# Performance work log

Hardware: AMD Instinct MI355X
Metric: run time of the kernel (lower is better)

The kernel has to match this reference:

```python
import jax, jax.numpy as jnp
import numpy as np

# Multi-scale feature pyramid (static: determines per-level slice bounds)
SPATIAL_SHAPES = np.array([[100, 100], [50, 50], [25, 25], [13, 13], [7, 7]])  # (H, W) per level
LEVEL_START = np.concatenate([[0], np.cumsum(SPATIAL_SHAPES[:, 0] * SPATIAL_SHAPES[:, 1])])[:-1]
C = 256       # hidden_inplanes
HEADS = 8     # head_nums
POINTS = 4    # point_nums
LEVELS = 5    # feature_level_nums
FF = 2048     # feedforward_planes
DH = C // HEADS


def setup_inputs() -> dict:
    key = jax.random.key(0)
    ks = jax.random.split(key, 16)
    B = 2
    L = int((SPATIAL_SHAPES[:, 0] * SPATIAL_SHAPES[:, 1]).sum())  # 13343 tokens
    s = 0.02
    return {
        'src': jax.random.normal(ks[0], (B, L, C), jnp.float32),
        'pos': jax.random.normal(ks[1], (B, L, C), jnp.float32) * 0.1,
        'reference_points': jax.random.uniform(ks[2], (B, L, LEVELS, 2), jnp.float32),
        'wv': jax.random.normal(ks[3], (C, C), jnp.float32) * s,
        'bv': jnp.zeros((C,), jnp.float32),
        'wo': jax.random.normal(ks[4], (C, HEADS * LEVELS * POINTS * 2), jnp.float32) * s,
        'bo': jax.random.normal(ks[5], (HEADS * LEVELS * POINTS * 2,), jnp.float32) * 0.5,
        'wa': jax.random.normal(ks[6], (C, HEADS * LEVELS * POINTS), jnp.float32) * s,
        'ba': jnp.zeros((HEADS * LEVELS * POINTS,), jnp.float32),
        'wout': jax.random.normal(ks[7], (C, C), jnp.float32) * s,
        'bout': jnp.zeros((C,), jnp.float32),
        'ln1g': jnp.ones((C,), jnp.float32),
        'ln1b': jnp.zeros((C,), jnp.float32),
        'w1': jax.random.normal(ks[8], (C, FF), jnp.float32) * s,
        'b1': jnp.zeros((FF,), jnp.float32),
        'w2': jax.random.normal(ks[9], (FF, C), jnp.float32) * s,
        'b2': jnp.zeros((C,), jnp.float32),
        'ln2g': jnp.ones((C,), jnp.float32),
        'ln2b': jnp.zeros((C,), jnp.float32),
    }


def layernorm(x, g, b, eps=1e-5):
    m = jnp.mean(x, -1, keepdims=True)
    v = jnp.var(x, -1, keepdims=True)
    return (x - m) * jax.lax.rsqrt(v + eps) * g + b


def bilinear_sample(val, loc, Hs, Ws):
    # val: [B, heads, H*W, dh]   loc: [B, heads, Lq, P, 2] normalized coords in [0,1]
    # grid_sample semantics, align_corners=False, zero padding outside
    px = loc[..., 0] * Ws - 0.5
    py = loc[..., 1] * Hs - 0.5
    x0 = jnp.floor(px); y0 = jnp.floor(py)
    lx = px - x0;       ly = py - y0
    x0i = x0.astype(jnp.int32); y0i = y0.astype(jnp.int32)
    gather = jax.vmap(jax.vmap(lambda v, i: v[i]))  # over batch, head dims
    out = jnp.zeros(loc.shape[:-1] + (val.shape[-1],), val.dtype)
    for dx, dy, w in ((0, 0, (1 - lx) * (1 - ly)), (1, 0, lx * (1 - ly)),
                      (0, 1, (1 - lx) * ly), (1, 1, lx * ly)):
        xi = x0i + dx; yi = y0i + dy
        valid = (xi >= 0) & (xi < Ws) & (yi >= 0) & (yi < Hs)
        idx = jnp.clip(yi, 0, Hs - 1) * Ws + jnp.clip(xi, 0, Ws - 1)
        g = gather(val, idx)  # [B, heads, Lq, P, dh]
        out = out + (w * valid)[..., None] * g
    return out


def msdeform_attn(query, value_in, ref, wv, bv, wo, bo, wa, ba, wout, bout):
    B, Lq, _ = query.shape
    # value projection -> [B, heads, Len, dh]
    value = (value_in @ wv + bv).reshape(B, -1, HEADS, DH).transpose(0, 2, 1, 3)
    offsets = (query @ wo + bo).reshape(B, Lq, HEADS, LEVELS, POINTS, 2)
    attn = jax.nn.softmax((query @ wa + ba).reshape(B, Lq, HEADS, LEVELS * POINTS), -1)
    attn = attn.reshape(B, Lq, HEADS, LEVELS, POINTS)
    # offset normalizer = (W, H) per level
    norml = jnp.asarray(SPATIAL_SHAPES[:, ::-1].copy(), jnp.float32)
    loc = ref[:, :, None, :, None, :] + offsets / norml[None, None, None, :, None, :]
    acc = jnp.zeros((B, Lq, HEADS, DH), query.dtype)
    for l in range(LEVELS):
        Hs, Ws = int(SPATIAL_SHAPES[l, 0]), int(SPATIAL_SHAPES[l, 1])
        s = int(LEVEL_START[l])
        vl = value[:, :, s:s + Hs * Ws, :]
        locl = jnp.transpose(loc[:, :, :, l], (0, 2, 1, 3, 4))  # [B, heads, Lq, P, 2]
        samp = bilinear_sample(vl, locl, Hs, Ws)                 # [B, heads, Lq, P, dh]
        acc = acc + jnp.einsum('bhqpd,bqhp->bqhd', samp, attn[:, :, :, l])
    return acc.reshape(B, Lq, C) @ wout + bout


def reference(src, pos, reference_points, wv, bv, wo, bo, wa, ba, wout, bout,
              ln1g, ln1b, w1, b1, w2, b2, ln2g, ln2b):
    # DeformableTransformerEncoderLayer (eval mode, dropout off)
    q = src + pos
    src2 = msdeform_attn(q, src, reference_points, wv, bv, wo, bo, wa, ba, wout, bout)
    x = layernorm(src + src2, ln1g, ln1b)
    ffn = jax.nn.relu(x @ w1 + b1) @ w2 + b2
    return layernorm(x + ffn, ln2g, ln2b)
```

## Files before the change

kernel.cpp:

```cpp
#include <hip/hip_runtime.h>
#include <hip/hip_bf16.h>

typedef __hip_bfloat16 bf16;
typedef unsigned short ushort_t;
typedef __attribute__((ext_vector_type(8))) short bf16x8;
typedef __attribute__((ext_vector_type(16))) float f32x16;

__device__ __forceinline__ float us2f(unsigned short u) {
    unsigned int x = ((unsigned int)u) << 16;
    return __uint_as_float(x);
}
__device__ __forceinline__ ushort_t f2us(float f) {
    return ((__hip_bfloat16_raw)__float2bfloat16(f)).x;
}

__device__ __forceinline__ void gl_lds16(const ushort_t* g, ushort_t* l) {
    __builtin_amdgcn_global_load_lds(
        (const __attribute__((address_space(1))) void*)g,
        (__attribute__((address_space(3))) void*)l, 16, 0, 0);
}

template<bool RELU, bool OUT_BF16, bool HAS_RESID>
__device__ __forceinline__ void epi_store_tile(
    float* __restrict__ tl, const f32x16& acc, int lane,
    int mbase, int nbase, const float* __restrict__ bias,
    const float* __restrict__ resid, void* __restrict__ outv, int M, int N)
{
    const int l32 = lane & 31, hi = lane >> 5;
    #pragma unroll
    for (int r = 0; r < 16; ++r) {
        const int row = (r & 3) + ((r >> 2) << 3) + hi * 4;
        tl[row * 34 + l32] = acc[r];
    }
    const int rr = lane >> 1;
    const int cc = (lane & 1) * 16;
    const int m  = mbase + rr;
    const int nb = nbase + cc;
    if (m >= M || nb >= N) return;

    if (OUT_BF16) {
        bf16* op = (bf16*)outv + (size_t)m * N + nb;
        #pragma unroll
        for (int gv = 0; gv < 2; ++gv) {
            unsigned pk[4];
            #pragma unroll
            for (int q = 0; q < 2; ++q) {
                const int c = cc + gv * 8 + q * 4;
                const float4 v  = *reinterpret_cast<const float4*>(&tl[rr * 34 + c]);
                const float4 b4 = *reinterpret_cast<const float4*>(&bias[nbase + c]);
                float o0 = v.x + b4.x, o1 = v.y + b4.y;
                float o2 = v.z + b4.z, o3 = v.w + b4.w;
                if (HAS_RESID) {
                    const float4 r4 = *reinterpret_cast<const float4*>(
                        &resid[(size_t)m * N + nbase + c]);
                    o0 += r4.x; o1 += r4.y; o2 += r4.z; o3 += r4.w;
                }
                if (RELU) {
                    o0 = fmaxf(o0, 0.f); o1 = fmaxf(o1, 0.f);
                    o2 = fmaxf(o2, 0.f); o3 = fmaxf(o3, 0.f);
                }
                pk[q * 2 + 0] = (unsigned)f2us(o0) | ((unsigned)f2us(o1) << 16);
                pk[q * 2 + 1] = (unsigned)f2us(o2) | ((unsigned)f2us(o3) << 16);
            }
            int4 w4; w4.x = pk[0]; w4.y = pk[1]; w4.z = pk[2]; w4.w = pk[3];
            *reinterpret_cast<int4*>(op + gv * 8) = w4;
        }
    } else {
        float* op = (float*)outv + (size_t)m * N + nb;
        #pragma unroll
        for (int q = 0; q < 4; ++q) {
            const int c = cc + q * 4;
            const float4 v  = *reinterpret_cast<const float4*>(&tl[rr * 34 + c]);
            const float4 b4 = *reinterpret_cast<const float4*>(&bias[nbase + c]);
            float4 o;
            o.x = v.x + b4.x; o.y = v.y + b4.y;
            o.z = v.z + b4.z; o.w = v.w + b4.w;
            if (HAS_RESID) {
                const float4 r4 = *reinterpret_cast<const float4*>(
                    &resid[(size_t)m * N + nbase + c]);
                o.x += r4.x; o.y += r4.y; o.z += r4.z; o.w += r4.w;
            }
            if (RELU) {
                o.x = fmaxf(o.x, 0.f); o.y = fmaxf(o.y, 0.f);
                o.z = fmaxf(o.z, 0.f); o.w = fmaxf(o.w, 0.f);
            }
            *reinterpret_cast<float4*>(op + q * 4) = o;
        }
    }
}

__global__ __launch_bounds__(256) void cast2_kernel(
    const float* __restrict__ src, const float* __restrict__ pos,
    bf16* __restrict__ src_b, bf16* __restrict__ q_b, int n)
{
    int i = (blockIdx.x * 256 + threadIdx.x) * 4;
    if (i < n) {
        const float4 s4 = *reinterpret_cast<const float4*>(&src[i]);
        const float4 p4 = *reinterpret_cast<const float4*>(&pos[i]);
        int2 sp, qp;
        sp.x = (unsigned)f2us(s4.x) | ((unsigned)f2us(s4.y) << 16);
        sp.y = (unsigned)f2us(s4.z) | ((unsigned)f2us(s4.w) << 16);
        qp.x = (unsigned)f2us(s4.x + p4.x) | ((unsigned)f2us(s4.y + p4.y) << 16);
        qp.y = (unsigned)f2us(s4.z + p4.z) | ((unsigned)f2us(s4.w + p4.w) << 16);
        *reinterpret_cast<int2*>((ushort_t*)src_b + i) = sp;
        *reinterpret_cast<int2*>((ushort_t*)q_b + i) = qp;
    }
}

__global__ __launch_bounds__(256) void prep_kernel(
    const float* __restrict__ wv, const float* __restrict__ wo,
    const float* __restrict__ wa, const float* __restrict__ wout,
    const float* __restrict__ w1, const float* __restrict__ w2,
    const float* __restrict__ bo, const float* __restrict__ ba,
    bf16* __restrict__ wvt, bf16* __restrict__ wcat, bf16* __restrict__ woutt,
    bf16* __restrict__ w1t, bf16* __restrict__ w2t, float* __restrict__ bcat)
{
    __shared__ float tile[32][33];
    const int b = blockIdx.x;
    const float* W; bf16* Wt; int K, N, tb;
    if (b < 64)        { W = wv;   Wt = wvt;            K = 256;  N = 256;  tb = b; }
    else if (b < 144)  { W = wo;   Wt = wcat;           K = 256;  N = 320;  tb = b - 64; }
    else if (b < 184)  { W = wa;   Wt = wcat + 320*256; K = 256;  N = 160;  tb = b - 144; }
    else if (b < 248)  { W = wout; Wt = woutt;          K = 256;  N = 256;  tb = b - 184; }
    else if (b < 760)  { W = w1;   Wt = w1t;            K = 256;  N = 2048; tb = b - 248; }
    else if (b < 1272) { W = w2;   Wt = w2t;            K = 2048; N = 256;  tb = b - 760; }
    else {
        int i = (b - 1272) * 256 + threadIdx.x;
        if (i < 320) bcat[i] = bo[i];
        else if (i < 480) bcat[i] = ba[i - 320];
        return;
    }
    const int ntn = N >> 5;
    const int nb = (tb % ntn) * 32, kb = (tb / ntn) * 32;
    const int tx = threadIdx.x & 31, ty = threadIdx.x >> 5;
    #pragma unroll
    for (int i = 0; i < 32; i += 8) {
        int k = kb + ty + i, n = nb + tx;
        tile[ty + i][tx] = (k < K && n < N) ? W[(size_t)k * N + n] : 0.f;
    }
    __syncthreads();
    #pragma unroll
    for (int i = 0; i < 32; i += 8) {
        int n = nb + ty + i, k = kb + tx;
        if (n < N && k < K)
            Wt[(size_t)n * K + k] = __float2bfloat16(tile[tx][ty + i]);
    }
}

template<bool RELU, bool OUT_BF16, bool HAS_RESID>
__global__ __launch_bounds__(256, 4) void gemm_mfma(
    const ushort_t* __restrict__ A,
    const ushort_t* __restrict__ Bt,
    const float* __restrict__ bias,
    const float* __restrict__ resid,
    void* __restrict__ outv, int M, int N, int K)
{
    __shared__ ushort_t Asmem[128 * 32];
    __shared__ ushort_t Bsmem[128 * 32];
    __shared__ float tlds[4][32 * 34];
    const int tid = threadIdx.x;
    const int lane = tid & 63;
    const int wave = tid >> 6;
    const int l32 = lane & 31;
    const int hi  = lane >> 5;
    const int wm = wave >> 1, wn = wave & 1;
    const int m0 = blockIdx.y * 128;
    const int n0 = blockIdx.x * 128;

    const int srow = lane >> 2;
    const int sch  = (lane & 3) * 8;

    const ushort_t* aP[2]; const ushort_t* bP[2];
    ushort_t* aL[2]; ushort_t* bL[2];
    #pragma unroll
    for (int i = 0; i < 2; ++i) {
        const int rbase = wave * 32 + i * 16;
        int mA = m0 + rbase + srow; if (mA > M - 1) mA = M - 1;
        int nB = n0 + rbase + srow; if (nB > N - 1) nB = N - 1;
        aP[i] = A  + (size_t)mA * K + sch;
        bP[i] = Bt + (size_t)nB * K + sch;
        aL[i] = &Asmem[rbase * 32];
        bL[i] = &Bsmem[rbase * 32];
    }

    f32x16 acc[2][2] = {};

    for (int k0 = 0; k0 < K; k0 += 32) {
        #pragma unroll
        for (int i = 0; i < 2; ++i) {
            gl_lds16(aP[i], aL[i]);
            gl_lds16(bP[i], bL[i]);
            aP[i] += 32; bP[i] += 32;
        }
        __syncthreads();

        #pragma unroll
        for (int kw = 0; kw < 2; ++kw) {
            bf16x8 af[2], bfr[2];
            #pragma unroll
            for (int i = 0; i < 2; ++i) {
                const int rowA = wm * 64 + i * 32 + l32;
                af[i] = *reinterpret_cast<const bf16x8*>(
                    &Asmem[rowA * 32 + kw * 16 + hi * 8]);
                const int rowB = wn * 64 + i * 32 + l32;
                bfr[i] = *reinterpret_cast<const bf16x8*>(
                    &Bsmem[rowB * 32 + kw * 16 + hi * 8]);
            }
            #pragma unroll
            for (int i = 0; i < 2; ++i)
                #pragma unroll
                for (int j = 0; j < 2; ++j)
                    acc[i][j] = __builtin_amdgcn_mfma_f32_32x32x16_bf16(
                        af[i], bfr[j], acc[i][j], 0, 0, 0);
        }
        __syncthreads();
    }

    float* tl = &tlds[wave][0];
    #pragma unroll
    for (int i = 0; i < 2; ++i)
        #pragma unroll
        for (int j = 0; j < 2; ++j)
            epi_store_tile<RELU, OUT_BF16, HAS_RESID>(
                tl, acc[i][j], lane,
                m0 + wm * 64 + i * 32, n0 + wn * 64 + j * 32,
                bias, resid, outv, M, N);
}

template<bool RELU, bool OUT_BF16, bool HAS_RESID>
__global__ __launch_bounds__(256, 4) void gemm_mfma_s(
    const ushort_t* __restrict__ A,
    const ushort_t* __restrict__ Bt,
    const float* __restrict__ bias,
    const float* __restrict__ resid,
    void* __restrict__ outv, int M, int N, int K)
{
    __shared__ ushort_t Asmem[64 * 32];
    __shared__ ushort_t Bsmem[128 * 32];
    const int tid = threadIdx.x;
    const int lane = tid & 63;
    const int wave = tid >> 6;
    const int l32 = lane & 31;
    const int hi  = lane >> 5;
    const int wm = wave >> 1;
    const int wn = wave & 1;
    const int m0 = blockIdx.y * 64;
    const int n0 = blockIdx.x * 128;

    const int srow = lane >> 2;
    const int sch  = (lane & 3) * 8;

    int mA = m0 + wave * 16 + srow; if (mA > M - 1) mA = M - 1;
    const ushort_t* aP = A + (size_t)mA * K + sch;
    ushort_t* aL = &Asmem[(wave * 16) * 32];
    const ushort_t* bP[2]; ushort_t* bL[2];
    #pragma unroll
    for (int i = 0; i < 2; ++i) {
        const int rbase = wave * 32 + i * 16;
        int nB = n0 + rbase + srow; if (nB > N - 1) nB = N - 1;
        bP[i] = Bt + (size_t)nB * K + sch;
        bL[i] = &Bsmem[rbase * 32];
    }

    f32x16 acc[2] = {};

    for (int k0 = 0; k0 < K; k0 += 32) {
        gl_lds16(aP, aL);       aP    += 32;
        gl_lds16(bP[0], bL[0]); bP[0] += 32;
        gl_lds16(bP[1], bL[1]); bP[1] += 32;
        __syncthreads();

        #pragma unroll
        for (int kw = 0; kw < 2; ++kw) {
            const bf16x8 af = *reinterpret_cast<const bf16x8*>(
                &Asmem[(wm * 32 + l32) * 32 + kw * 16 + hi * 8]);
            bf16x8 bfr[2];
            #pragma unroll
            for (int j = 0; j < 2; ++j) {
                const int rowB = wn * 64 + j * 32 + l32;
                bfr[j] = *reinterpret_cast<const bf16x8*>(
                    &Bsmem[rowB * 32 + kw * 16 + hi * 8]);
            }
            #pragma unroll
            for (int j = 0; j < 2; ++j)
                acc[j] = __builtin_amdgcn_mfma_f32_32x32x16_bf16(
                    af, bfr[j], acc[j], 0, 0, 0);
        }
        __syncthreads();
    }

    const int mb = m0 + wm * 32 + hi * 4;
    #pragma unroll
    for (int j = 0; j < 2; ++j) {
        const int n = n0 + wn * 64 + j * 32 + l32;
        if (n >= N) continue;
        const float bval = bias[n];
        #pragma unroll
        for (int r = 0; r < 16; ++r) {
            const int m = mb + (r & 3) + (r >> 2) * 8;
            if (m >= M) continue;
            float v = acc[j][r] + bval;
            if (HAS_RESID) v += resid[(size_t)m * N + n];
            if (RELU) v = fmaxf(v, 0.f);
            if (OUT_BF16)
                ((bf16*)outv)[(size_t)m * N + n] = __float2bfloat16(v);
            else
                ((float*)outv)[(size_t)m * N + n] = v;
        }
    }
}

__global__ __launch_bounds__(256) void msda_kernel_v3(
    const ushort_t* __restrict__ og,
    const float* __restrict__ refp,
    const ushort_t* __restrict__ value,
    bf16* __restrict__ out,
    int M, int L)
{
    const int tid = threadIdx.x;
    const int qbase = blockIdx.x * 8;

    __shared__ float  s_attn[8][160];
    __shared__ int2   s_off[1280];
    __shared__ float4 s_w[1280];
    __shared__ int    s_Wl[5], s_St[5];

    if (tid < 5) {
        const int HW[5] = {100, 50, 25, 13, 7};
        const int st[5] = {0, 10000, 12500, 13125, 13294};
        s_Wl[tid] = HW[tid];
        s_St[tid] = st[tid];
    }

    for (int i = tid; i < 1280; i += 256) {
        int q = i / 160, j = i - q * 160;
        int qq = qbase + q;
        s_attn[q][j] = (qq < M) ? us2f(og[(size_t)qq * 480 + 320 + j]) : 0.f;
    }
    __syncthreads();

    if (tid < 64) {
        float* a = &s_attn[tid >> 3][(tid & 7) * 20];
        float mx = -1e30f;
        #pragma unroll
        for (int i = 0; i < 20; ++i) mx = fmaxf(mx, a[i]);
        float ssum = 0.f;
        #pragma unroll
        for (int i = 0; i < 20; ++i) {
            float e = __expf(a[i] - mx);
            a[i] = e;
            ssum += e;
        }
        float inv = 1.f / ssum;
        #pragma unroll
        for (int i = 0; i < 20; ++i) a[i] *= inv;
    }
    __syncthreads();

    #pragma unroll
    for (int it = 0; it < 5; ++it) {
        const int t = tid + it * 256;
        const int q  = t / 160;
        const int r  = t - q * 160;
        const int l  = (r - (r / 20) * 20) >> 2;
        const int qq = qbase + q;

        int2 offp = {0, 0};
        float4 wp = {0.f, 0.f, 0.f, 0.f};
        if (qq < M) {
            const int Wi = s_Wl[l];
            const int s0 = s_St[l];
            const float Wf = (float)Wi;
            const float ox = us2f(og[(size_t)qq * 480 + r * 2]);
            const float oy = us2f(og[(size_t)qq * 480 + r * 2 + 1]);
            const float2 rf = *reinterpret_cast<const float2*>(
                &refp[(size_t)qq * 10 + l * 2]);
            const float a = s_attn[q][r];

            const float px = fmaf(rf.x, Wf, -0.5f) + ox;
            const float py = fmaf(rf.y, Wf, -0.5f) + oy;
            const float x0f = floorf(px);
            const float y0f = floorf(py);
            const float lx = px - x0f;
            const float ly = py - y0f;
            const int x0 = (int)x0f;
            const int y0 = (int)y0f;

            const float wx0v = (x0 >= 0 && x0 < Wi) ? (1.f - lx) : 0.f;
            const float wx1v = (x0 + 1 >= 0 && x0 + 1 < Wi) ? lx : 0.f;
            const float wy0v = (y0 >= 0 && y0 < Wi) ? (1.f - ly) : 0.f;
            const float wy1v = (y0 + 1 >= 0 && y0 + 1 < Wi) ? ly : 0.f;

            const int c0 = min(max(x0, 0), Wi - 2);
            const int r0 = min(max(y0, 0), Wi - 2);
            const float swx0 = (x0 == c0 ? wx0v : 0.f) + (x0 + 1 == c0 ? wx1v : 0.f);
            const float swx1 = (x0 == c0 + 1 ? wx0v : 0.f) + (x0 + 1 == c0 + 1 ? wx1v : 0.f);
            const float swy0 = (y0 == r0 ? wy0v : 0.f) + (y0 + 1 == r0 ? wy1v : 0.f);
            const float swy1 = (y0 == r0 + 1 ? wy0v : 0.f) + (y0 + 1 == r0 + 1 ? wy1v : 0.f);

            offp.x = (s0 + r0 * Wi + c0) * 512;
            offp.y = offp.x + Wi * 512;
            wp.x = a * swx0 * swy0;
            wp.y = a * swx1 * swy0;
            wp.z = a * swx0 * swy1;
            wp.w = a * swx1 * swy1;
        }
        s_off[t] = offp;
        s_w[t] = wp;
    }
    __syncthreads();

    const int qi  = tid >> 5;
    const int g   = tid & 31;
    const int h   = g >> 2;
    const int sub = g & 3;
    const int bq = qbase + qi;
    if (bq >= M) return;
    const int b = bq / L;

    const char* vb = (const char*)value + (size_t)b * L * 512 + h * 64 + sub * 16;

    float acc[8] = {};
    const int tb = qi * 160 + h * 20;
    #pragma unroll 2
    for (int p = 0; p < 20; ++p) {
        const int2 off = s_off[tb + p];
        const float4 w = s_w[tb + p];
        const int4 u00 = *reinterpret_cast<const int4*>(vb + off.x);
        const int4 u10 = *reinterpret_cast<const int4*>(vb + off.x + 512);
        const int4 u01 = *reinterpret_cast<const int4*>(vb + off.y);
        const int4 u11 = *reinterpret_cast<const int4*>(vb + off.y + 512);
        #define ACC4(u, wt)                                                        \
            acc[0] = fmaf(wt, __uint_as_float((unsigned)(u).x << 16), acc[0]);      \
            acc[1] = fmaf(wt, __uint_as_float((unsigned)(u).x & 0xffff0000u), acc[1]); \
            acc[2] = fmaf(wt, __uint_as_float((unsigned)(u).y << 16), acc[2]);      \
            acc[3] = fmaf(wt, __uint_as_float((unsigned)(u).y & 0xffff0000u), acc[3]); \
            acc[4] = fmaf(wt, __uint_as_float((unsigned)(u).z << 16), acc[4]);      \
            acc[5] = fmaf(wt, __uint_as_float((unsigned)(u).z & 0xffff0000u), acc[5]); \
            acc[6] = fmaf(wt, __uint_as_float((unsigned)(u).w << 16), acc[6]);      \
            acc[7] = fmaf(wt, __uint_as_float((unsigned)(u).w & 0xffff0000u), acc[7]);
        ACC4(u00, w.x)
        ACC4(u10, w.y)
        ACC4(u01, w.z)
        ACC4(u11, w.w)
        #undef ACC4
    }

    ushort_t o[8];
    #pragma unroll
    for (int i = 0; i < 8; ++i) o[i] = f2us(acc[i]);
    int4 pkt;
    pkt.x = (int)o[0] | ((int)o[1] << 16);
    pkt.y = (int)o[2] | ((int)o[3] << 16);
    pkt.z = (int)o[4] | ((int)o[5] << 16);
    pkt.w = (int)o[6] | ((int)o[7] << 16);
    *reinterpret_cast<int4*>((ushort_t*)out + (size_t)bq * 256 + h * 32 + sub * 8) = pkt;
}

template<bool DUAL>
__global__ __launch_bounds__(256) void ln_kernel(
    const float* __restrict__ y, const float* __restrict__ g,
    const float* __restrict__ bta, float* __restrict__ outf,
    bf16* __restrict__ outb, int M)
{
    const int wave = threadIdx.x >> 6, lane = threadIdx.x & 63;
    const int row = blockIdx.x * 4 + wave;
    if (row >= M) return;
    const float4 v = *reinterpret_cast<const float4*>(&y[(size_t)row * 256 + lane * 4]);
    float s  = v.x + v.y + v.z + v.w;
    float ss = v.x * v.x + v.y * v.y + v.z * v.z + v.w * v.w;
    #pragma unroll
    for (int o = 32; o > 0; o >>= 1) {
        s += __shfl_down(s, o);
        ss += __shfl_down(ss, o);
    }
    s = __shfl(s, 0);
    ss = __shfl(ss, 0);
    const float mean = s * (1.f / 256.f);
    const float var = ss * (1.f / 256.f) - mean * mean;
    const float rs = rsqrtf(var + 1e-5f);
    const float4 g4 = *reinterpret_cast<const float4*>(&g[lane * 4]);
    const float4 b4 = *reinterpret_cast<const float4*>(&bta[lane * 4]);
    float4 o4;
    o4.x = (v.x - mean) * rs * g4.x + b4.x;
    o4.y = (v.y - mean) * rs * g4.y + b4.y;
    o4.z = (v.z - mean) * rs * g4.z + b4.z;
    o4.w = (v.w - mean) * rs * g4.w + b4.w;
    *reinterpret_cast<float4*>(&outf[(size_t)row * 256 + lane * 4]) = o4;
    if (DUAL) {
        int2 pk;
        pk.x = (unsigned)f2us(o4.x) | ((unsigned)f2us(o4.y) << 16);
        pk.y = (unsigned)f2us(o4.z) | ((unsigned)f2us(o4.w) << 16);
        *reinterpret_cast<int2*>((ushort_t*)outb + (size_t)row * 256 + lane * 4) = pk;
    }
}

extern "C" void kernel_launch(void* const* d_in, const int* in_sizes, int n_in,
                              void* d_out, int out_size, void* d_ws, size_t ws_size,
                              hipStream_t stream)
{
    const int B = 2, L = 13343, C = 256, FF = 2048;
    const int M = B * L;

    const float* src  = (const float*)d_in[0];
    const float* pos  = (const float*)d_in[1];
    const float* refp = (const float*)d_in[2];
    const float* wv   = (const float*)d_in[3];
    const float* bv   = (const float*)d_in[4];
    const float* wo   = (const float*)d_in[5];
    const float* bo   = (const float*)d_in[6];
    const float* wa   = (const float*)d_in[7];
    const float* ba   = (const float*)d_in[8];
    const float* wout = (const float*)d_in[9];
    const float* bout = (const float*)d_in[10];
    const float* ln1g = (const float*)d_in[11];
    const float* ln1b = (const float*)d_in[12];
    const float* w1   = (const float*)d_in[13];
    const float* b1   = (const float*)d_in[14];
    const float* w2   = (const float*)d_in[15];
    const float* b2   = (const float*)d_in[16];
    const float* ln2g = (const float*)d_in[17];
    const float* ln2b = (const float*)d_in[18];

    char* ws = (char*)d_ws;
    const size_t MB = 1ull << 20;
    bf16*  src_b  = (bf16*)(ws + 0);
    bf16*  q_b    = (bf16*)(ws + 14 * MB);
    bf16*  val_b  = (bf16*)(ws + 28 * MB);
    bf16*  og     = (bf16*)(ws + 42 * MB);
    bf16*  acc_b  = (bf16*)(ws + 95 * MB);
    bf16*  h_b    = (bf16*)(ws + 0);
    float* y      = (float*)(ws + 110 * MB);
    float* z      = (float*)(ws + 110 * MB);
    bf16*  x_b    = (bf16*)(ws + 138 * MB);
    float* x_f    = (float*)(ws + 152 * MB);
    bf16* wvt    = (bf16*)(ws + 180 * MB);
    bf16* wcat   = wvt + 256 * 256;
    bf16* woutt  = wcat + 480 * 256;
    bf16* w1t    = woutt + 256 * 256;
    bf16* w2t    = w1t + 2048 * 256;
    float* bcat  = (float*)(w2t + 256 * 2048);
    (void)ws_size; (void)n_in; (void)in_sizes; (void)out_size;

    const int mt   = (M + 127) / 128;
    const int mt64 = (M + 63) / 64;
    const int lnb  = (M + 3) / 4;

    prep_kernel<<<1274, 256, 0, stream>>>(wv, wo, wa, wout, w1, w2, bo, ba,
                                          wvt, wcat, woutt, w1t, w2t, bcat);

    cast2_kernel<<<(M * C / 4 + 255) / 256, 256, 0, stream>>>(
        src, pos, src_b, q_b, M * C);

    gemm_mfma_s<false, true, false><<<dim3(2, mt64), 256, 0, stream>>>(
        (const ushort_t*)src_b, (const ushort_t*)wvt, bv, nullptr, val_b, M, 256, 256);

    gemm_mfma<false, true, false><<<dim3(4, mt), 256, 0, stream>>>(
        (const ushort_t*)q_b, (const ushort_t*)wcat, bcat, nullptr, og, M, 480, 256);

    msda_kernel_v3<<<(M + 7) / 8, 256, 0, stream>>>(
        (const ushort_t*)og, refp, (const ushort_t*)val_b, acc_b, M, L);

    gemm_mfma_s<false, false, true><<<dim3(2, mt64), 256, 0, stream>>>(
        (const ushort_t*)acc_b, (const ushort_t*)woutt, bout, src, y, M, 256, 256);

    ln_kernel<true><<<lnb, 256, 0, stream>>>(y, ln1g, ln1b, x_f, x_b, M);

    gemm_mfma<true, true, false><<<dim3(16, mt), 256, 0, stream>>>(
        (const ushort_t*)x_b, (const ushort_t*)w1t, b1, nullptr, h_b, M, FF, 256);

    gemm_mfma_s<false, false, true><<<dim3(2, mt64), 256, 0, stream>>>(
        (const ushort_t*)h_b, (const ushort_t*)w2t, b2, x_f, z, M, 256, FF);

    ln_kernel<false><<<lnb, 256, 0, stream>>>(z, ln2g, ln2b, (float*)d_out, nullptr, M);
}
```

Before: 410.7 us.

## Store pre-LayerNorm activations in bf16 and remap small-GEMM grid for L2 locality

The output-projection and FFN2 GEMMs now write their pre-LayerNorm sums as bf16 instead of fp32. The LayerNorm kernels read bf16 and either emit bf16 or the final fp32 output. The fp32 copy x_f is dropped, and the FFN residual is taken from the bf16 x_b. This roughly halves the activation traffic across these stages at the cost of extra bf16 rounding in the residual path. The narrow-N GEMM also moves to a 1D grid in which pairs of N-tiles sharing the same M rows are grouped in runs of 8 row tiles, so A rows are reused from cache.

```diff
diff --git a/kernel.cpp b/kernel.cpp
--- a/kernel.cpp
+++ b/kernel.cpp
@@ -227,16 +227,23 @@
                 bias, resid, outv, M, N);
 }
 
-template<bool RELU, bool OUT_BF16, bool HAS_RESID>
+template<bool RELU, bool OUT_BF16, bool HAS_RESID, bool RESID_BF16>
 __global__ __launch_bounds__(256, 4) void gemm_mfma_s(
     const ushort_t* __restrict__ A,
     const ushort_t* __restrict__ Bt,
     const float* __restrict__ bias,
-    const float* __restrict__ resid,
-    void* __restrict__ outv, int M, int N, int K)
+    const void* __restrict__ residv,
+    void* __restrict__ outv, int M, int N, int K, int mtiles)
 {
     __shared__ ushort_t Asmem[64 * 32];
     __shared__ ushort_t Bsmem[128 * 32];
+    const int lid = blockIdx.x;
+    const int xb = (lid >> 3) & 1;
+    const int yg = ((lid >> 4) << 3) | (lid & 7);
+    if (yg >= mtiles) return;
+    const int m0 = yg * 64;
+    const int n0 = xb * 128;
+
     const int tid = threadIdx.x;
     const int lane = tid & 63;
     const int wave = tid >> 6;
@@ -244,8 +251,6 @@
     const int hi  = lane >> 5;
     const int wm = wave >> 1;
     const int wn = wave & 1;
-    const int m0 = blockIdx.y * 64;
-    const int n0 = blockIdx.x * 128;
 
     const int srow = lane >> 2;
     const int sch  = (lane & 3) * 8;
@@ -300,7 +305,12 @@
             const int m = mb + (r & 3) + (r >> 2) * 8;
             if (m >= M) continue;
             float v = acc[j][r] + bval;
-            if (HAS_RESID) v += resid[(size_t)m * N + n];
+            if (HAS_RESID) {
+                if (RESID_BF16)
+                    v += us2f(((const ushort_t*)residv)[(size_t)m * N + n]);
+                else
+                    v += ((const float*)residv)[(size_t)m * N + n];
+            }
             if (RELU) v = fmaxf(v, 0.f);
             if (OUT_BF16)
                 ((bf16*)outv)[(size_t)m * N + n] = __float2bfloat16(v);
@@ -457,18 +467,21 @@
     *reinterpret_cast<int4*>((ushort_t*)out + (size_t)bq * 256 + h * 32 + sub * 8) = pkt;
 }
 
-template<bool DUAL>
+template<bool OUT_BF16>
 __global__ __launch_bounds__(256) void ln_kernel(
-    const float* __restrict__ y, const float* __restrict__ g,
-    const float* __restrict__ bta, float* __restrict__ outf,
-    bf16* __restrict__ outb, int M)
+    const ushort_t* __restrict__ yb, const float* __restrict__ g,
+    const float* __restrict__ bta, void* __restrict__ outv, int M)
 {
     const int wave = threadIdx.x >> 6, lane = threadIdx.x & 63;
     const int row = blockIdx.x * 4 + wave;
     if (row >= M) return;
-    const float4 v = *reinterpret_cast<const float4*>(&y[(size_t)row * 256 + lane * 4]);
-    float s  = v.x + v.y + v.z + v.w;
-    float ss = v.x * v.x + v.y * v.y + v.z * v.z + v.w * v.w;
+    const int2 raw = *reinterpret_cast<const int2*>(&yb[(size_t)row * 256 + lane * 4]);
+    float v0 = us2f((ushort_t)((unsigned)raw.x & 0xffffu));
+    float v1 = us2f((ushort_t)((unsigned)raw.x >> 16));
+    float v2 = us2f((ushort_t)((unsigned)raw.y & 0xffffu));
+    float v3 = us2f((ushort_t)((unsigned)raw.y >> 16));
+    float s  = v0 + v1 + v2 + v3;
+    float ss = v0 * v0 + v1 * v1 + v2 * v2 + v3 * v3;
     #pragma unroll
     for (int o = 32; o > 0; o >>= 1) {
         s += __shfl_down(s, o);
@@ -482,16 +495,17 @@
     const float4 g4 = *reinterpret_cast<const float4*>(&g[lane * 4]);
     const float4 b4 = *reinterpret_cast<const float4*>(&bta[lane * 4]);
     float4 o4;
-    o4.x = (v.x - mean) * rs * g4.x + b4.x;
-    o4.y = (v.y - mean) * rs * g4.y + b4.y;
-    o4.z = (v.z - mean) * rs * g4.z + b4.z;
-    o4.w = (v.w - mean) * rs * g4.w + b4.w;
-    *reinterpret_cast<float4*>(&outf[(size_t)row * 256 + lane * 4]) = o4;
-    if (DUAL) {
+    o4.x = (v0 - mean) * rs * g4.x + b4.x;
+    o4.y = (v1 - mean) * rs * g4.y + b4.y;
+    o4.z = (v2 - mean) * rs * g4.z + b4.z;
+    o4.w = (v3 - mean) * rs * g4.w + b4.w;
+    if (OUT_BF16) {
         int2 pk;
         pk.x = (unsigned)f2us(o4.x) | ((unsigned)f2us(o4.y) << 16);
         pk.y = (unsigned)f2us(o4.z) | ((unsigned)f2us(o4.w) << 16);
-        *reinterpret_cast<int2*>((ushort_t*)outb + (size_t)row * 256 + lane * 4) = pk;
+        *reinterpret_cast<int2*>((ushort_t*)outv + (size_t)row * 256 + lane * 4) = pk;
+    } else {
+        *reinterpret_cast<float4*>((float*)outv + (size_t)row * 256 + lane * 4) = o4;
     }
 }
 
@@ -530,11 +544,10 @@
     bf16*  og     = (bf16*)(ws + 42 * MB);
     bf16*  acc_b  = (bf16*)(ws + 95 * MB);
     bf16*  h_b    = (bf16*)(ws + 0);
-    float* y      = (float*)(ws + 110 * MB);
-    float* z      = (float*)(ws + 110 * MB);
+    bf16*  y      = (bf16*)(ws + 110 * MB);
+    bf16*  z      = (bf16*)(ws + 110 * MB);
     bf16*  x_b    = (bf16*)(ws + 138 * MB);
-    float* x_f    = (float*)(ws + 152 * MB);
-    bf16* wvt    = (bf16*)(ws + 180 * MB);
+    bf16* wvt    = (bf16*)(ws + 152 * MB);
     bf16* wcat   = wvt + 256 * 256;
     bf16* woutt  = wcat + 480 * 256;
     bf16* w1t    = woutt + 256 * 256;
@@ -542,9 +555,10 @@
     float* bcat  = (float*)(w2t + 256 * 2048);
     (void)ws_size; (void)n_in; (void)in_sizes; (void)out_size;
 
-    const int mt   = (M + 127) / 128;
-    const int mt64 = (M + 63) / 64;
-    const int lnb  = (M + 3) / 4;
+    const int mt    = (M + 127) / 128;
+    const int mt64  = (M + 63) / 64;
+    const int sgrid = ((mt64 + 7) / 8) * 16;
+    const int lnb   = (M + 3) / 4;
 
     prep_kernel<<<1274, 256, 0, stream>>>(wv, wo, wa, wout, w1, w2, bo, ba,
                                           wvt, wcat, woutt, w1t, w2t, bcat);
@@ -552,8 +566,9 @@
     cast2_kernel<<<(M * C / 4 + 255) / 256, 256, 0, stream>>>(
         src, pos, src_b, q_b, M * C);
 
-    gemm_mfma_s<false, true, false><<<dim3(2, mt64), 256, 0, stream>>>(
-        (const ushort_t*)src_b, (const ushort_t*)wvt, bv, nullptr, val_b, M, 256, 256);
+    gemm_mfma_s<false, true, false, false><<<sgrid, 256, 0, stream>>>(
+        (const ushort_t*)src_b, (const ushort_t*)wvt, bv, nullptr, val_b,
+        M, 256, 256, mt64);
 
     gemm_mfma<false, true, false><<<dim3(4, mt), 256, 0, stream>>>(
         (const ushort_t*)q_b, (const ushort_t*)wcat, bcat, nullptr, og, M, 480, 256);
@@ -561,16 +576,20 @@
     msda_kernel_v3<<<(M + 7) / 8, 256, 0, stream>>>(
         (const ushort_t*)og, refp, (const ushort_t*)val_b, acc_b, M, L);
 
-    gemm_mfma_s<false, false, true><<<dim3(2, mt64), 256, 0, stream>>>(
-        (const ushort_t*)acc_b, (const ushort_t*)woutt, bout, src, y, M, 256, 256);
-
-    ln_kernel<true><<<lnb, 256, 0, stream>>>(y, ln1g, ln1b, x_f, x_b, M);
+    gemm_mfma_s<false, true, true, false><<<sgrid, 256, 0, stream>>>(
+        (const ushort_t*)acc_b, (const ushort_t*)woutt, bout, src, y,
+        M, 256, 256, mt64);
+
+    ln_kernel<true><<<lnb, 256, 0, stream>>>(
+        (const ushort_t*)y, ln1g, ln1b, x_b, M);
 
     gemm_mfma<true, true, false><<<dim3(16, mt), 256, 0, stream>>>(
         (const ushort_t*)x_b, (const ushort_t*)w1t, b1, nullptr, h_b, M, FF, 256);
 
-    gemm_mfma_s<false, false, true><<<dim3(2, mt64), 256, 0, stream>>>(
-        (const ushort_t*)h_b, (const ushort_t*)w2t, b2, x_f, z, M, 256, FF);
-
-    ln_kernel<false><<<lnb, 256, 0, stream>>>(z, ln2g, ln2b, (float*)d_out, nullptr, M);
-}
+    gemm_mfma_s<false, true, true, true><<<sgrid, 256, 0, stream>>>(
+        (const ushort_t*)h_b, (const ushort_t*)w2t, b2, x_b, z,
+        M, 256, FF, mt64);
+
+    ln_kernel<false><<<lnb, 256, 0, stream>>>(
+        (const ushort_t*)z, ln2g, ln2b, (float*)d_out, M);
+}
```

Result: faster. 399.0 us (-2.9%).
